# Optimization experiments

Measured on AMD Instinct MI355X. Metric: run time of the kernel, lower is better.

## Reference

```python
import jax, jax.numpy as jnp
import numpy as np

T, B, F, H = 256, 128, 1024, 1024  # time (orig dim0), batch (orig dim1), input, hidden


def _xavier(key, shape):
    fan_in, fan_out = shape
    limit = float(np.sqrt(6.0 / (fan_in + fan_out)))
    return jax.random.uniform(key, shape, jnp.float32, -limit, limit)


def setup_inputs() -> dict:
    key = jax.random.key(0)
    k1, k2, k3 = jax.random.split(key, 3)
    return {
        "x": jax.random.normal(k1, (T, B, F), dtype=jnp.float32),
        "h0": jnp.zeros((H,), jnp.float32),
        "c0": jnp.zeros((H,), jnp.float32),
        "weight_ih": _xavier(k2, (F, 4 * H)),
        "weight_hh": _xavier(k3, (H, 4 * H)),
        "bias": jnp.zeros((4 * H,), jnp.float32),
    }


def reference(x, h0, c0, weight_ih, weight_hh, bias):
    # Faithful to the torch code: due to its transpose+index quirk, the
    # recurrence runs over the ORIGINAL dim 0 (time=T) with dim 1 as batch.
    hs = H
    h_init = jnp.broadcast_to(h0, (B, hs))
    c_init = jnp.broadcast_to(c0, (B, hs))

    def step(carry, x_t):  # x_t: (B, F)
        h, c = carry
        gates = x_t @ weight_ih + h @ weight_hh + bias  # (B, 4H)
        i = jax.nn.sigmoid(gates[:, :hs])
        f = jax.nn.sigmoid(gates[:, hs:2 * hs])
        g = jnp.tanh(gates[:, 2 * hs:3 * hs])
        o = jax.nn.sigmoid(gates[:, 3 * hs:])
        c_new = f * c + i * g
        h_new = o * jnp.tanh(c_new)
        return (h_new, c_new), h_new

    (h_t, c_t), hidden_seq = jax.lax.scan(step, (h_init, c_init), x)
    return hidden_seq, h_t, c_t  # hidden_seq: (T, B, H)
```

## Files before the change

kernel.cpp:

```cpp
#include <hip/hip_runtime.h>
#include <hip/hip_bf16.h>


typedef __attribute__((ext_vector_type(8))) short short8;
typedef __attribute__((ext_vector_type(4))) float floatx4;

#define HID_OFF 33554432L
#define CT_OFF  33685504L
#define WTAIL_F 29360128L

__device__ __forceinline__ unsigned short f2bf(float f) {
    __hip_bfloat16 hb = __float2bfloat16(f);
    return *reinterpret_cast<unsigned short*>(&hb);
}

__device__ __forceinline__ uint4 pack8(const float* p) {
    float4 f0 = *reinterpret_cast<const float4*>(p);
    float4 f1 = *reinterpret_cast<const float4*>(p + 4);
    union { uint4 v; unsigned short u[8]; } t;
    t.u[0] = f2bf(f0.x); t.u[1] = f2bf(f0.y); t.u[2] = f2bf(f0.z); t.u[3] = f2bf(f0.w);
    t.u[4] = f2bf(f1.x); t.u[5] = f2bf(f1.y); t.u[6] = f2bf(f1.z); t.u[7] = f2bf(f1.w);
    return t.v;
}

__global__ void pack_w_kernel(const float* __restrict__ wih,
                              const float* __restrict__ whh,
                              unsigned short* __restrict__ pB) {
    int g    = blockIdx.x * 256 + threadIdx.x;
    int lane = g & 63;
    int frag = g >> 6;
    int kblk = frag & 63;
    int nblk = frag >> 6;
    int n = nblk * 16 + (lane & 15);
    int k = kblk * 32 + ((lane >> 4) << 3);
    const float* src = (k < 1024) ? (wih + (size_t)k * 4096 + n)
                                  : (whh + (size_t)(k - 1024) * 4096 + n);
    __attribute__((aligned(16))) unsigned short tmp[8];
#pragma unroll
    for (int jj = 0; jj < 8; ++jj) tmp[jj] = f2bf(src[(size_t)jj * 4096]);
    *reinterpret_cast<uint4*>(pB + (size_t)frag * 512 + lane * 8) =
        *reinterpret_cast<const uint4*>(tmp);
}

__global__ void pack_x_kernel(const float* __restrict__ x,
                              unsigned short* __restrict__ pX) {
    int g    = blockIdx.x * 256 + threadIdx.x;
    int lane = g & 63;
    int frag = g >> 6;
    int kblk = frag & 31;
    int mblk = (frag >> 5) & 7;
    int t    = frag >> 8;
    int m = mblk * 16 + (lane & 15);
    int k = kblk * 32 + ((lane >> 4) << 3);
    *reinterpret_cast<uint4*>(pX + (size_t)frag * 512 + lane * 8) =
        pack8(x + (size_t)(t * 128 + m) * 1024 + k);
}

__global__ __launch_bounds__(256, 1) void lstm_main(
    const float* __restrict__ x, const float* __restrict__ h0,
    const float* __restrict__ c0, const float* __restrict__ bias,
    const unsigned short* __restrict__ pB,
    unsigned short* pH, int use_ph,
    const unsigned short* __restrict__ pX, int use_px,
    float* out, int* cnt) {

    __shared__ __align__(16) unsigned short AbufX[2][32][512];
    __shared__ __align__(16) unsigned short AbufH[2][32][512];
    __shared__ float g_lds[4][32][17];
    __shared__ float c_lds[32][16];
    __shared__ __align__(16) unsigned short hbf_lds[32][16];

    const int tid  = threadIdx.x;
    const int lane = tid & 63;
    const int w    = tid >> 6;
    const int wg   = blockIdx.x;
    const int r    = (wg >> 3) & 3;
    const int j    = (wg & 7) * 8 + (wg >> 5);
    const int col  = lane & 15;
    const int quad = lane >> 4;
    const int nblk = w * 64 + j;

    int* subp = cnt + (r * 8 + (j >> 3)) * 64;

    const float breg = bias[w * 1024 + j * 16 + col];

    {
        float cv = c0[j * 16 + (tid & 15)];
        int row = tid >> 4;
        c_lds[row][tid & 15]      = cv;
        c_lds[row + 16][tid & 15] = cv;
    }

    const unsigned short* pBw = pB + (size_t)nblk * 64 * 512 + lane * 8;
    short8 bw[64];
#pragma unroll
    for (int kb = 0; kb < 64; ++kb)
        bw[kb] = *reinterpret_cast<const short8*>(pBw + (size_t)kb * 512);

    auto stage_x_full = [&](int tt) {
#pragma unroll
        for (int i = 0; i < 16; ++i) {
            int s = tid + 256 * i;
            int ln = s & 63, kbg = (s >> 6) & 31, mb = s >> 11;
            if (use_px) {
                const unsigned short* src =
                    pX + (((size_t)(tt * 8 + 2 * r + mb) * 32 + kbg) * 512) + ln * 8;
                *reinterpret_cast<uint4*>(&AbufX[mb][kbg][ln * 8]) =
                    *reinterpret_cast<const uint4*>(src);
            } else {
                int m = 32 * r + mb * 16 + (ln & 15);
                int k = kbg * 32 + ((ln >> 4) << 3);
                *reinterpret_cast<uint4*>(&AbufX[mb][kbg][ln * 8]) =
                    pack8(x + (size_t)(tt * 128 + m) * 1024 + k);
            }
        }
    };

    auto stage_h0 = [&]() {
#pragma unroll
        for (int i = 0; i < 16; ++i) {
            int s = tid + 256 * i;
            int ln = s & 63, kbg = (s >> 6) & 31, mb = s >> 11;
            int k = kbg * 32 + ((ln >> 4) << 3);
            union { uint4 v; unsigned short u[8]; } tv;
#pragma unroll
            for (int jj = 0; jj < 8; ++jj) tv.u[jj] = f2bf(h0[k + jj]);
            *reinterpret_cast<uint4*>(&AbufH[mb][kbg][ln * 8]) = tv.v;
        }
    };

    auto stage_h_out = [&](int tt) {
#pragma unroll
        for (int i = 0; i < 16; ++i) {
            int s = tid + 256 * i;
            int ln = s & 63, kbg = (s >> 6) & 31, mb = s >> 11;
            int m = 32 * r + mb * 16 + (ln & 15);
            int k = kbg * 32 + ((ln >> 4) << 3);
            *reinterpret_cast<uint4*>(&AbufH[mb][kbg][ln * 8]) =
                pack8(out + (size_t)(tt - 1) * 131072 + (size_t)m * 1024 + k);
        }
    };

    auto gemm_x = [&](floatx4& A0, floatx4& A1) {
#pragma unroll
        for (int kb = 0; kb < 32; ++kb) {
            short8 a0 = *reinterpret_cast<const short8*>(&AbufX[0][kb][lane * 8]);
            short8 a1 = *reinterpret_cast<const short8*>(&AbufX[1][kb][lane * 8]);
            A0 = __builtin_amdgcn_mfma_f32_16x16x32_bf16(a0, bw[kb], A0, 0, 0, 0);
            A1 = __builtin_amdgcn_mfma_f32_16x16x32_bf16(a1, bw[kb], A1, 0, 0, 0);
        }
    };
    auto gemm_h = [&](floatx4& A0, floatx4& A1) {
#pragma unroll
        for (int kb = 0; kb < 32; ++kb) {
            short8 a0 = *reinterpret_cast<const short8*>(&AbufH[0][kb][lane * 8]);
            short8 a1 = *reinterpret_cast<const short8*>(&AbufH[1][kb][lane * 8]);
            A0 = __builtin_amdgcn_mfma_f32_16x16x32_bf16(a0, bw[32 + kb], A0, 0, 0, 0);
            A1 = __builtin_amdgcn_mfma_f32_16x16x32_bf16(a1, bw[32 + kb], A1, 0, 0, 0);
        }
    };

    __syncthreads();
    stage_x_full(0);
    asm volatile("s_waitcnt lgkmcnt(0)" ::: "memory");
    __builtin_amdgcn_s_barrier();

    for (int t = 0; t < 256; ++t) {
        if (t > 0 && tid < 8) {
            int* sp = cnt + (r * 8 + tid) * 64;
            const int target = 8 * t;
            while (true) {
                int vv = __hip_atomic_load(sp, __ATOMIC_RELAXED,
                                           __HIP_MEMORY_SCOPE_AGENT);
                if (__ballot(vv >= target) == 0xFFull) break;
                __builtin_amdgcn_s_sleep(1);
            }
            if (!use_ph)
                __builtin_amdgcn_fence(__ATOMIC_ACQUIRE, "agent");
        }
        __builtin_amdgcn_s_barrier();

        uint4 hreg[16];
        if (t == 0) {
            stage_h0();
        } else if (use_ph) {
            const char* bb = (const char*)pH + (size_t)(t & 1) * 262144 +
                             (size_t)r * 65536 + (tid >> 6) * 1024 + (tid & 63) * 16;
#pragma unroll
            for (int i = 0; i < 16; ++i)
                asm volatile("global_load_dwordx4 %0, %1, off sc0 sc1"
                             : "=v"(hreg[i]) : "v"(bb + (size_t)i * 4096) : "memory");
        } else {
            stage_h_out(t);
        }

        floatx4 acc0 = {0.f, 0.f, 0.f, 0.f}, acc1 = {0.f, 0.f, 0.f, 0.f};
        gemm_x(acc0, acc1);

        if (t > 0 && use_ph) {
            __builtin_amdgcn_sched_barrier(0);
            asm volatile("s_waitcnt vmcnt(0)" ::: "memory");
            __builtin_amdgcn_sched_barrier(0);
            unsigned short* ld = &AbufH[0][0][0] + (tid >> 6) * 512 + (tid & 63) * 8;
#pragma unroll
            for (int i = 0; i < 16; ++i)
                *reinterpret_cast<uint4*>(ld + i * 2048) = hreg[i];
        }
        __syncthreads();

        gemm_h(acc0, acc1);

#pragma unroll
        for (int rr = 0; rr < 4; ++rr) {
            float p0 = acc0[rr] + breg;
            float p1 = acc1[rr] + breg;
            float v0, v1;
            if (w == 2) { v0 = tanhf(p0); v1 = tanhf(p1); }
            else        { v0 = 1.f / (1.f + __expf(-p0)); v1 = 1.f / (1.f + __expf(-p1)); }
            g_lds[w][quad * 4 + rr][col]      = v0;
            g_lds[w][16 + quad * 4 + rr][col] = v1;
        }
        __syncthreads();

        const int row0 = tid >> 4, cc = tid & 15;
        float hv0, hv1, cn0, cn1;
        {
            float iv = g_lds[0][row0][cc];
            float fv = g_lds[1][row0][cc];
            float gv = g_lds[2][row0][cc];
            float ov = g_lds[3][row0][cc];
            cn0 = fv * c_lds[row0][cc] + iv * gv;
            hv0 = ov * tanhf(cn0);
            c_lds[row0][cc]   = cn0;
            hbf_lds[row0][cc] = f2bf(hv0);
            int row1 = row0 + 16;
            iv = g_lds[0][row1][cc];
            fv = g_lds[1][row1][cc];
            gv = g_lds[2][row1][cc];
            ov = g_lds[3][row1][cc];
            cn1 = fv * c_lds[row1][cc] + iv * gv;
            hv1 = ov * tanhf(cn1);
            c_lds[row1][cc]   = cn1;
            hbf_lds[row1][cc] = f2bf(hv1);
        }
        __syncthreads();

        auto store_out = [&]() {
            const long hidbase = (long)t * 131072;
            const long m0 = 32 * r + row0, m1 = m0 + 16;
            out[hidbase + m0 * 1024 + j * 16 + cc] = hv0;
            out[hidbase + m1 * 1024 + j * 16 + cc] = hv1;
            if (t == 255) {
                out[HID_OFF + m0 * 1024 + j * 16 + cc] = hv0;
                out[HID_OFF + m1 * 1024 + j * 16 + cc] = hv1;
                out[CT_OFF  + m0 * 1024 + j * 16 + cc] = cn0;
                out[CT_OFF  + m1 * 1024 + j * 16 + cc] = cn1;
            }
        };

        if (!use_ph) store_out();

        if (t < 255) {
            if (use_ph && tid < 64) {
                int ml = tid >> 1, cg = tid & 1;
                int m = 32 * r + ml, kcol = j * 16 + cg * 8;
                int frag  = (2 * r + (ml >> 4)) * 32 + (kcol >> 5);
                int lanep = (m & 15) + 16 * ((kcol & 31) >> 3);
                unsigned short* dst = pH + (size_t)((t & 1) ^ 1) * 131072 +
                                      (size_t)frag * 512 + lanep * 8;
                const unsigned long long* sv =
                    reinterpret_cast<const unsigned long long*>(&hbf_lds[ml][cg * 8]);
                unsigned long long* d64 = reinterpret_cast<unsigned long long*>(dst);
                __hip_atomic_store(d64, sv[0], __ATOMIC_RELAXED,
                                   __HIP_MEMORY_SCOPE_AGENT);
                __hip_atomic_store(d64 + 1, sv[1], __ATOMIC_RELAXED,
                                   __HIP_MEMORY_SCOPE_AGENT);
            }
            if (tid == 0) {
                if (use_ph) {
                    asm volatile("s_waitcnt vmcnt(0)" ::: "memory");
                    __hip_atomic_fetch_add(subp, 1, __ATOMIC_RELAXED,
                                           __HIP_MEMORY_SCOPE_AGENT);
                } else {
                    __hip_atomic_fetch_add(subp, 1, __ATOMIC_RELEASE,
                                           __HIP_MEMORY_SCOPE_AGENT);
                }
            }
        }

        if (use_ph) store_out();

        if (t < 255) stage_x_full(t + 1);
        asm volatile("s_waitcnt lgkmcnt(0)" ::: "memory");
        __builtin_amdgcn_s_barrier();
    }
}

extern "C" void kernel_launch(void* const* d_in, const int* in_sizes, int n_in,
                              void* d_out, int out_size, void* d_ws, size_t ws_size,
                              hipStream_t stream) {
    (void)in_sizes; (void)n_in; (void)out_size;
    const float* x    = (const float*)d_in[0];
    const float* h0   = (const float*)d_in[1];
    const float* c0   = (const float*)d_in[2];
    const float* wih  = (const float*)d_in[3];
    const float* whh  = (const float*)d_in[4];
    const float* bias = (const float*)d_in[5];
    float* out = (float*)d_out;

    char* ws = (char*)d_ws;
    int* counters = (int*)ws;
    const size_t SZB = 2048ull * 4096 * 2;
    const size_t SZH = 2ull * 256 * 512 * 2;
    const size_t SZX = 65536ull * 512 * 2;

    size_t off = 16384;
    unsigned short* pB;
    if (ws_size >= off + SZB) {
        pB = (unsigned short*)(ws + off); off += SZB;
    } else {
        pB = (unsigned short*)(out + WTAIL_F);
    }
    int use_ph = (ws_size >= off + SZH) ? 1 : 0;
    unsigned short* pH = use_ph ? (unsigned short*)(ws + off) : (unsigned short*)0;
    if (use_ph) off += SZH;
    int use_px = (ws_size >= off + SZX) ? 1 : 0;
    unsigned short* pX = use_px ? (unsigned short*)(ws + off) : (unsigned short*)0;

    hipMemsetAsync(ws, 0, 16384, stream);
    pack_w_kernel<<<4096, 256, 0, stream>>>(wih, whh, pB);
    if (use_px) pack_x_kernel<<<16384, 256, 0, stream>>>(x, pX);

    lstm_main<<<dim3(256), dim3(256), 0, stream>>>(
        x, h0, c0, bias, pB, pH, use_ph, pX, use_px, out, counters);
}
```

Baseline: 3.203 ms.

## Add per-XCD leader refresh so h-state loads can use L2-cached reads

```diff
diff --git a/kernel.cpp b/kernel.cpp
--- a/kernel.cpp
+++ b/kernel.cpp
@@ -69,6 +69,7 @@
     __shared__ float g_lds[4][32][17];
     __shared__ float c_lds[32][16];
     __shared__ __align__(16) unsigned short hbf_lds[32][16];
+    __shared__ int amp_lds[3];
 
     const int tid  = threadIdx.x;
     const int lane = tid & 63;
@@ -91,11 +92,43 @@
         c_lds[row + 16][tid & 15] = cv;
     }
 
+    if (use_ph && tid == 0) {
+        int xcc;
+        asm volatile("s_getreg_b32 %0, hwreg(20, 0, 32)" : "=s"(xcc));
+        xcc &= 7;
+        int rk = __hip_atomic_fetch_add(cnt + 3072 + xcc, 1, __ATOMIC_RELAXED,
+                                        __HIP_MEMORY_SCOPE_AGENT);
+        amp_lds[0] = xcc;
+        amp_lds[1] = rk;
+        if (rk == 0) {
+            *(volatile int*)(cnt + 3200 + xcc * 64) = 0x5EED0 + xcc;
+            asm volatile("s_waitcnt vmcnt(0)" ::: "memory");
+        }
+        __hip_atomic_fetch_add(cnt + 3840, 1, __ATOMIC_RELAXED,
+                               __HIP_MEMORY_SCOPE_AGENT);
+    }
+
     const unsigned short* pBw = pB + (size_t)nblk * 64 * 512 + lane * 8;
     short8 bw[64];
 #pragma unroll
     for (int kb = 0; kb < 64; ++kb)
         bw[kb] = *reinterpret_cast<const short8*>(pBw + (size_t)kb * 512);
+
+    if (use_ph && tid == 0) {
+        while (__hip_atomic_load(cnt + 3840, __ATOMIC_RELAXED,
+                                 __HIP_MEMORY_SCOPE_AGENT) < 256)
+            __builtin_amdgcn_s_sleep(1);
+        int probe, xcc = amp_lds[0];
+        asm volatile("global_load_dword %0, %1, off sc0\n"
+                     "s_waitcnt vmcnt(0)"
+                     : "=v"(probe) : "v"(cnt + 3200 + xcc * 64) : "memory");
+        amp_lds[2] = (probe == 0x5EED0 + xcc) ? 1 : 0;
+    } else if (tid == 0) {
+        amp_lds[0] = 0; amp_lds[1] = 1; amp_lds[2] = 0;
+    }
+    __syncthreads();
+    const int  xcd     = amp_lds[0];
+    const bool is_lead = (use_ph != 0) && (amp_lds[1] == 0);
 
     auto stage_x_full = [&](int tt) {
 #pragma unroll
@@ -160,36 +193,68 @@
         }
     };
 
-    __syncthreads();
     stage_x_full(0);
     asm volatile("s_waitcnt lgkmcnt(0)" ::: "memory");
     __builtin_amdgcn_s_barrier();
 
     for (int t = 0; t < 256; ++t) {
-        if (t > 0 && tid < 8) {
-            int* sp = cnt + (r * 8 + tid) * 64;
-            const int target = 8 * t;
-            while (true) {
-                int vv = __hip_atomic_load(sp, __ATOMIC_RELAXED,
-                                           __HIP_MEMORY_SCOPE_AGENT);
-                if (__ballot(vv >= target) == 0xFFull) break;
-                __builtin_amdgcn_s_sleep(1);
-            }
-            if (!use_ph)
-                __builtin_amdgcn_fence(__ATOMIC_ACQUIRE, "agent");
+        const int parity = t & 1;
+
+        if (t > 0) {
+            if (tid < 8) {
+                int* sp = cnt + (r * 8 + tid) * 64;
+                const int target = 8 * t;
+                while (true) {
+                    int vv = __hip_atomic_load(sp, __ATOMIC_RELAXED,
+                                               __HIP_MEMORY_SCOPE_AGENT);
+                    if (__ballot(vv >= target) == 0xFFull) break;
+                    __builtin_amdgcn_s_sleep(1);
+                }
+                if (!use_ph)
+                    __builtin_amdgcn_fence(__ATOMIC_ACQUIRE, "agent");
+            }
+            if (tid == 0) {
+                if (is_lead) {
+                    __builtin_amdgcn_fence(__ATOMIC_ACQUIRE, "agent");
+                    asm volatile("s_waitcnt vmcnt(0)" ::: "memory");
+                    *(volatile int*)(cnt + 2048 + xcd * 64) = t;
+                    asm volatile("s_waitcnt vmcnt(0)" ::: "memory");
+                }
+                if (amp_lds[2]) {
+                    const int* fp = cnt + 2048 + xcd * 64;
+                    int fv, spins = 0;
+                    while (true) {
+                        asm volatile("global_load_dword %0, %1, off sc0\n"
+                                     "s_waitcnt vmcnt(0)"
+                                     : "=v"(fv) : "v"(fp) : "memory");
+                        if (fv >= t) break;
+                        if (++spins > (1 << 15)) { amp_lds[2] = 0; break; }
+                        __builtin_amdgcn_s_sleep(1);
+                    }
+                    asm volatile("s_waitcnt lgkmcnt(0)" ::: "memory");
+                }
+            }
         }
         __builtin_amdgcn_s_barrier();
+        const int l2m = amp_lds[2];
 
         uint4 hreg[16];
         if (t == 0) {
             stage_h0();
         } else if (use_ph) {
-            const char* bb = (const char*)pH + (size_t)(t & 1) * 262144 +
-                             (size_t)r * 65536 + (tid >> 6) * 1024 + (tid & 63) * 16;
-#pragma unroll
-            for (int i = 0; i < 16; ++i)
-                asm volatile("global_load_dwordx4 %0, %1, off sc0 sc1"
-                             : "=v"(hreg[i]) : "v"(bb + (size_t)i * 4096) : "memory");
+            const char* bb2 = (const char*)pH + (size_t)parity * 262144 +
+                              (size_t)r * 65536 + (size_t)tid * 16;
+            if (l2m) {
+#pragma unroll
+                for (int i = 0; i < 16; ++i)
+                    asm volatile("global_load_dwordx4 %0, %1, off sc0"
+                                 : "=v"(hreg[i]) : "v"(bb2 + (size_t)i * 4096) : "memory");
+            } else {
+#pragma unroll
+                for (int i = 0; i < 16; ++i)
+                    asm volatile("global_load_dwordx4 %0, %1, off sc0 sc1"
+                                 : "=v"(hreg[i]) : "v"(bb2 + (size_t)i * 4096) : "memory");
+            }
         } else {
             stage_h_out(t);
         }
@@ -201,7 +266,7 @@
             __builtin_amdgcn_sched_barrier(0);
             asm volatile("s_waitcnt vmcnt(0)" ::: "memory");
             __builtin_amdgcn_sched_barrier(0);
-            unsigned short* ld = &AbufH[0][0][0] + (tid >> 6) * 512 + (tid & 63) * 8;
+            unsigned short* ld = &AbufH[0][0][0] + tid * 8;
 #pragma unroll
             for (int i = 0; i < 16; ++i)
                 *reinterpret_cast<uint4*>(ld + i * 2048) = hreg[i];
@@ -266,7 +331,7 @@
                 int m = 32 * r + ml, kcol = j * 16 + cg * 8;
                 int frag  = (2 * r + (ml >> 4)) * 32 + (kcol >> 5);
                 int lanep = (m & 15) + 16 * ((kcol & 31) >> 3);
-                unsigned short* dst = pH + (size_t)((t & 1) ^ 1) * 131072 +
+                unsigned short* dst = pH + (size_t)(parity ^ 1) * 131072 +
                                       (size_t)frag * 512 + lanep * 8;
                 const unsigned long long* sv =
                     reinterpret_cast<const unsigned long long*>(&hbf_lds[ml][cg * 8]);
```

Result: slower. 12.45 ms (+288.8%).
